# Kernel optimization log

Measured on AMD Instinct MI355X. Metric: run time of the kernel, lower is better.

Reference implementation:

```python
import jax, jax.numpy as jnp
import numpy as np

B, L, H, HKV, D, E = 2, 2048, 8, 1, 256, 2048
SCALING = D ** -0.5


def rotate_half(x):
    x1, x2 = jnp.split(x, 2, axis=-1)
    return jnp.concatenate([-x2, x1], axis=-1)


def setup_inputs() -> dict:
    key = jax.random.key(0)
    ks = jax.random.split(key, 5)
    hidden_states = jax.random.normal(ks[0], (B, L, E), jnp.float32)
    attention_mask = jnp.zeros((B, 1, 1, L, L), jnp.float32)  # additive mask (all visible)
    # standard RoPE tables, shape [L, D]
    inv_freq = 1.0 / (10000.0 ** (jnp.arange(0, D, 2, dtype=jnp.float32) / D))
    freqs = jnp.arange(L, dtype=jnp.float32)[:, None] * inv_freq[None, :]
    emb = jnp.concatenate([freqs, freqs], axis=-1)
    cos, sin = jnp.cos(emb), jnp.sin(emb)
    s = 0.02
    Wq = jax.random.normal(ks[1], (H * D, E), jnp.float32) * s
    Wk = jax.random.normal(ks[2], (HKV * D, E), jnp.float32) * s
    Wv = jax.random.normal(ks[3], (HKV * D, E), jnp.float32) * s
    Wo = jax.random.normal(ks[4], (E, H * D), jnp.float32) * s
    return {"hidden_states": hidden_states, "attention_mask": attention_mask,
            "cos": cos, "sin": sin, "Wq": Wq, "Wk": Wk, "Wv": Wv, "Wo": Wo}


def reference(hidden_states, attention_mask, cos, sin, Wq, Wk, Wv, Wo):
    b, l, _ = hidden_states.shape
    q = jnp.einsum('ble,de->bld', hidden_states, Wq)
    k = jnp.einsum('ble,de->bld', hidden_states, Wk)
    v = jnp.einsum('ble,de->bld', hidden_states, Wv)
    # q: [B, L, 1, H, D] -> transpose(1,3) -> [B, H, 1, L, D]
    q = jnp.transpose(q.reshape(b, l, 1, H, D), (0, 3, 2, 1, 4))
    # k, v: [B, 1, L, Hkv, D] -> transpose(2,3) -> [B, 1, Hkv, L, D]
    k = jnp.transpose(k.reshape(b, 1, l, HKV, D), (0, 1, 3, 2, 4))
    v = jnp.transpose(v.reshape(b, 1, l, HKV, D), (0, 1, 3, 2, 4))
    # RoPE (cos/sin broadcast over leading dims)
    q = q * cos + rotate_half(q) * sin
    k = k * cos + rotate_half(k) * sin
    # scores: [B, H, Hkv, L, L]
    attn = jnp.matmul(q, jnp.swapaxes(k, -1, -2)) * SCALING
    attn = attn + attention_mask
    attn = jax.nn.softmax(attn.astype(jnp.float32), axis=-1)
    out = jnp.matmul(attn, v)                         # [B, H, Hkv, L, D]
    out = jnp.transpose(out, (0, 1, 3, 2, 4))         # [B, H, L, Hkv, D]
    out = out.reshape(b, l, H * D)                    # row-major reshape, as torch .reshape
    return jnp.einsum('bld,ed->ble', out, Wo)
```

## Files before the change

### kernel.cpp

```cpp
#include <hip/hip_runtime.h>

typedef unsigned short u16;
typedef __attribute__((ext_vector_type(8))) short short8;
typedef __attribute__((ext_vector_type(4))) float f32x4;
typedef __attribute__((ext_vector_type(16))) float f32x16;

struct __align__(8) US4 { u16 x, y, z, w; };

__device__ __forceinline__ u16 f2bf(float x) {
  union { float f; unsigned u; } c; c.f = x;
  unsigned r = c.u + 0x7fffu + ((c.u >> 16) & 1u);
  return (u16)(r >> 16);
}
__device__ __forceinline__ float bf2f(u16 u) {
  union { unsigned u; float f; } c; c.u = ((unsigned)u) << 16;
  return c.f;
}
__device__ __forceinline__ void gload_lds16(const void* g, void* l) {
  __builtin_amdgcn_global_load_lds(
      (const __attribute__((address_space(1))) void*)g,
      (__attribute__((address_space(3))) void*)l, 16, 0, 0);
}
__device__ __forceinline__ f32x4 fzero4() {
  f32x4 z; z[0] = 0.f; z[1] = 0.f; z[2] = 0.f; z[3] = 0.f; return z;
}

__global__ __launch_bounds__(256) void cvt_all(
    const float* __restrict__ h, const float* __restrict__ wq,
    const float* __restrict__ wk, const float* __restrict__ wv,
    const float* __restrict__ wo, u16* __restrict__ Xbf,
    u16* __restrict__ Wqkv, u16* __restrict__ Wob) {
  int b = blockIdx.x;
  const float* s; u16* d; int off;
  if (b < 8192)       { s = h;  d = Xbf;            off = b; }
  else if (b < 12288) { s = wq; d = Wqkv;           off = b - 8192; }
  else if (b < 12800) { s = wk; d = Wqkv + 4194304; off = b - 12288; }
  else if (b < 13312) { s = wv; d = Wqkv + 4718592; off = b - 12800; }
  else                { s = wo; d = Wob;            off = b - 13312; }
  int i = (off * 256 + threadIdx.x) * 4;
  float4 v = *(const float4*)(s + i);
  US4 o = { f2bf(v.x), f2bf(v.y), f2bf(v.z), f2bf(v.w) };
  *(US4*)(d + i) = o;
}

template <int MODE>
__global__ __launch_bounds__(256) void gemm_nt(
    const u16* __restrict__ A, const u16* __restrict__ Bw,
    u16* __restrict__ q_out, u16* __restrict__ k_out, u16* __restrict__ v_out,
    float* __restrict__ c_out) {
  __shared__ u16 lA[128 * 32];
  __shared__ u16 lB[128 * 32];
  const int K = 2048;
  int t = threadIdx.x, w = t >> 6, lane = t & 63;
  int wm = w >> 1, wn = w & 1;
  int m0 = blockIdx.x * 128, n0 = blockIdx.y * 128;
  int g = lane >> 4, qi = lane & 15;

  f32x4 acc[4][4];
#pragma unroll
  for (int i = 0; i < 4; i++)
#pragma unroll
    for (int j = 0; j < 4; j++) acc[i][j] = fzero4();

  for (int k0 = 0; k0 < K; k0 += 32) {
#pragma unroll
    for (int i = 0; i < 2; i++) {
      int off = i * 4096 + w * 1024 + lane * 16;
      int row = off >> 6, cg = (off >> 4) & 3;
      gload_lds16(A + (size_t)(m0 + row) * K + k0 + cg * 8,
                  (char*)lA + i * 4096 + w * 1024);
      gload_lds16(Bw + (size_t)(n0 + row) * K + k0 + cg * 8,
                  (char*)lB + i * 4096 + w * 1024);
    }
    __syncthreads();
    short8 af[4], bfr[4];
#pragma unroll
    for (int f = 0; f < 4; f++) {
      int ra = wm * 64 + f * 16 + qi;
      int rb = wn * 64 + f * 16 + qi;
      int kb2 = g * 16;
      af[f] = *(const short8*)((const char*)lA + ra * 64 + kb2);
      bfr[f] = *(const short8*)((const char*)lB + rb * 64 + kb2);
    }
#pragma unroll
    for (int i = 0; i < 4; i++)
#pragma unroll
      for (int j = 0; j < 4; j++)
        acc[i][j] = __builtin_amdgcn_mfma_f32_16x16x32_bf16(af[i], bfr[j], acc[i][j], 0, 0, 0);
    __syncthreads();
  }

#pragma unroll
  for (int i = 0; i < 4; i++) {
#pragma unroll
    for (int j = 0; j < 4; j++) {
#pragma unroll
      for (int r = 0; r < 4; r++) {
        int m = m0 + wm * 64 + i * 16 + g * 4 + r;
        int n = n0 + wn * 64 + j * 16 + qi;
        float v = acc[i][j][r];
        if (MODE == 0) {
          int b = m >> 11, l = m & 2047;
          if (n < 2048) {
            int hh = n >> 8, dd = n & 255;
            q_out[(((size_t)(b * 8 + hh) * 2048) + l) * 256 + dd] = f2bf(v);
          } else if (n < 2304) {
            int dd = n - 2048;
            k_out[((size_t)b * 2048 + l) * 256 + dd] = f2bf(v);
          } else {
            int dd = n - 2304;
            v_out[((size_t)b * 256 + dd) * 2048 + l] = f2bf(v);
          }
        } else {
          c_out[(size_t)m * 2048 + n] = v;
        }
      }
    }
  }
}

__global__ __launch_bounds__(256) void rope_kernel(u16* __restrict__ q, u16* __restrict__ k,
                                                   const float* __restrict__ cosT,
                                                   const float* __restrict__ sinT) {
  int idx = blockIdx.x * 2 + (threadIdx.x >> 7);
  int d = threadIdx.x & 127;
  u16* ptr;
  int l;
  float sc;
  if (idx < 32768) { ptr = q + (size_t)idx * 256; l = idx & 2047; sc = 0.0625f; }
  else             { ptr = k + (size_t)(idx - 32768) * 256; l = (idx - 32768) & 2047; sc = 1.0f; }
  float x1 = bf2f(ptr[d]), x2 = bf2f(ptr[d + 128]);
  float c1 = cosT[l * 256 + d], s1 = sinT[l * 256 + d];
  float c2 = cosT[l * 256 + d + 128], s2 = sinT[l * 256 + d + 128];
  float o1 = (x1 * c1 - x2 * s1) * sc;
  float o2 = (x2 * c2 + x1 * s2) * sc;
  ptr[d] = f2bf(o1);
  ptr[d + 128] = f2bf(o2);
}

__global__ __launch_bounds__(512, 2) void flash_kernel(
    const u16* __restrict__ qr, const u16* __restrict__ kr,
    const u16* __restrict__ vt_g, u16* __restrict__ attnout) {
  __shared__ __align__(16) char lds[147456];

  int t = threadIdx.x, w = t >> 6, lane = t & 63;
  int lo5 = lane & 31, hi = lane >> 5;
  int half = w >> 2, wl = w & 3;
  int b = blockIdx.z, h = blockIdx.y;
  int bh = b * 8 + h;
  int l0 = blockIdx.x * 128;
  int qrow = l0 + wl * 32 + lo5;

  const u16* kb = kr + (size_t)b * (2048 * 256);
  const u16* vb = vt_g + (size_t)b * (256 * 2048);
  char* unitbase = lds + half * 65536;
  char* plw = lds + 131072 + w * 2048;
  int kvbase = half * 1024;

  short8 qf[16];
  {
    const u16* qb = qr + ((size_t)bh * 2048 + qrow) * 256 + hi * 8;
#pragma unroll
    for (int ks = 0; ks < 16; ks++) qf[ks] = *(const short8*)(qb + ks * 16);
  }

  f32x16 ot[8];
#pragma unroll
  for (int dv = 0; dv < 8; dv++)
#pragma unroll
    for (int r = 0; r < 16; r++) ot[dv][r] = 0.f;
  float mrow = -1e30f, lrow = 0.f;

  auto stage = [&](int buf, int it) {
    char* unit = unitbase + buf * 32768;
    int kvg = kvbase + it * 32;
#pragma unroll
    for (int i = 0; i < 4; i++) {
      int dbase = i * 4096 + wl * 1024;
      int off = dbase + lane * 16;
      {
        int row = off >> 9, slot = (off >> 4) & 31;
        int ss = slot ^ (row & 7);
        gload_lds16(kb + (size_t)(kvg + row) * 256 + ss * 8, unit + dbase);
      }
      {
        int dd = off >> 6, slot = (off >> 4) & 3;
        int ss = slot ^ ((dd >> 1) & 3);
        gload_lds16(vb + (size_t)dd * 2048 + kvg + ss * 8, unit + 16384 + dbase);
      }
    }
  };

  stage(0, 0);
  __syncthreads();

  for (int it = 0; it < 32; ++it) {
    int buf = it & 1;
    if (it < 31) stage(buf ^ 1, it + 1);
    char* unit = unitbase + buf * 32768;

    f32x16 st;
#pragma unroll
    for (int r = 0; r < 16; r++) st[r] = 0.f;
#pragma unroll
    for (int ks = 0; ks < 16; ks++) {
      int ss = (2 * ks + hi) ^ (lo5 & 7);
      short8 kf = *(const short8*)(unit + lo5 * 512 + ss * 16);
      st = __builtin_amdgcn_mfma_f32_32x32x16_bf16(kf, qf[ks], st, 0, 0, 0);
    }

    float tmax = st[0];
#pragma unroll
    for (int r = 1; r < 16; r++) tmax = fmaxf(tmax, st[r]);
    tmax = fmaxf(tmax, __shfl_xor(tmax, 32));
    if (__any(tmax > mrow)) {
      float mnew = fmaxf(mrow, tmax);
      float scale = __expf(mrow - mnew);
#pragma unroll
      for (int dv = 0; dv < 8; dv++)
#pragma unroll
        for (int r = 0; r < 16; r++) ot[dv][r] *= scale;
      lrow *= scale;
      mrow = mnew;
    }
    float tsum = 0.f;
#pragma unroll
    for (int r = 0; r < 16; r++) {
      float p = __expf(st[r] - mrow);
      st[r] = p;
      tsum += p;
    }
    tsum += __shfl_xor(tsum, 32);
    lrow += tsum;

#pragma unroll
    for (int r4 = 0; r4 < 4; r4++) {
      US4 pw = { f2bf(st[4 * r4 + 0]), f2bf(st[4 * r4 + 1]),
                 f2bf(st[4 * r4 + 2]), f2bf(st[4 * r4 + 3]) };
      int byte_ = lo5 * 64 + ((r4 ^ ((lo5 >> 1) & 3)) << 4) + hi * 8;
      *(US4*)(plw + byte_) = pw;
    }

#pragma unroll
    for (int jks = 0; jks < 2; jks++) {
      int ps = ((2 * jks + hi) ^ ((lo5 >> 1) & 3)) << 4;
      short8 pf = *(const short8*)(plw + lo5 * 64 + ps);
#pragma unroll
      for (int dv = 0; dv < 8; dv++) {
        int dd = dv * 32 + lo5;
        int ss = (2 * jks + hi) ^ ((dd >> 1) & 3);
        short8 vf = *(const short8*)(unit + 16384 + dd * 64 + ss * 16);
        ot[dv] = __builtin_amdgcn_mfma_f32_32x32x16_bf16(vf, pf, ot[dv], 0, 0, 0);
      }
    }
    __syncthreads();
  }

  char* chunk = lds + wl * 32768;
  float* mlx = (float*)(lds + 131072 + wl * 4096);
  if (half == 0) {
#pragma unroll
    for (int dv = 0; dv < 8; dv++)
#pragma unroll
      for (int r4 = 0; r4 < 4; r4++) {
        f32x4 v;
        v[0] = ot[dv][4 * r4 + 0]; v[1] = ot[dv][4 * r4 + 1];
        v[2] = ot[dv][4 * r4 + 2]; v[3] = ot[dv][4 * r4 + 3];
        *(f32x4*)(chunk + ((dv * 4 + r4) * 64 + lane) * 16) = v;
      }
    mlx[lane * 2 + 0] = mrow;
    mlx[lane * 2 + 1] = lrow;
  }
  __syncthreads();
  if (half == 1) {
    float mA = mlx[lane * 2 + 0], lA = mlx[lane * 2 + 1];
    float m = fmaxf(mA, mrow);
    float cA = __expf(mA - m), cB = __expf(mrow - m);
    float linv = 1.f / (lA * cA + lrow * cB);
    u16* ob = attnout + ((size_t)bh * 2048 + qrow) * 256;
#pragma unroll
    for (int dv = 0; dv < 8; dv++)
#pragma unroll
      for (int r4 = 0; r4 < 4; r4++) {
        f32x4 oA = *(const f32x4*)(chunk + ((dv * 4 + r4) * 64 + lane) * 16);
        US4 o;
        o.x = f2bf((oA[0] * cA + ot[dv][4 * r4 + 0] * cB) * linv);
        o.y = f2bf((oA[1] * cA + ot[dv][4 * r4 + 1] * cB) * linv);
        o.z = f2bf((oA[2] * cA + ot[dv][4 * r4 + 2] * cB) * linv);
        o.w = f2bf((oA[3] * cA + ot[dv][4 * r4 + 3] * cB) * linv);
        *(US4*)(ob + dv * 32 + 8 * r4 + 4 * hi) = o;
      }
  }
}

extern "C" void kernel_launch(void* const* d_in, const int* in_sizes, int n_in,
                              void* d_out, int out_size, void* d_ws, size_t ws_size,
                              hipStream_t stream) {
  const float* hidden = (const float*)d_in[0];
  const float* cosT = (const float*)d_in[2];
  const float* sinT = (const float*)d_in[3];
  const float* Wq = (const float*)d_in[4];
  const float* Wk = (const float*)d_in[5];
  const float* Wv = (const float*)d_in[6];
  const float* Wo = (const float*)d_in[7];

  char* ws = (char*)d_ws;
  u16* Xbf  = (u16*)(ws + 0);
  u16* Wqkv = (u16*)(ws + 16777216);
  u16* Wob  = (u16*)(ws + 27262976);
  u16* qbuf = (u16*)(ws + 35651584);
  u16* kbuf = (u16*)(ws + 52428800);
  u16* vT   = (u16*)(ws + 54525952);
  u16* attn = (u16*)(ws + 56623104);
  float* out = (float*)d_out;

  cvt_all<<<17408, 256, 0, stream>>>(hidden, Wq, Wk, Wv, Wo, Xbf, Wqkv, Wob);
  gemm_nt<0><<<dim3(32, 20), 256, 0, stream>>>(Xbf, Wqkv, qbuf, kbuf, vT, nullptr);
  rope_kernel<<<18432, 256, 0, stream>>>(qbuf, kbuf, cosT, sinT);
  flash_kernel<<<dim3(16, 8, 2), 512, 0, stream>>>(qbuf, kbuf, vT, attn);
  gemm_nt<1><<<dim3(32, 16), 256, 0, stream>>>(attn, Wob, nullptr, nullptr, nullptr, out);
}
```

Baseline: 281.0 us.

## Give each flash wave two query tiles and keep P in registers

The flash kernel now runs 4 waves per block instead of 8, and each wave handles two 32-row query tiles. Every K and V fragment read from LDS therefore feeds two MFMAs. The probability tile is converted to bf16 with packed converts and rearranged across lanes using permlane32 swaps, replacing the LDS write/read round trip. It also raises wave priority around the MFMA loops. In exchange, each wave holds twice as many accumulators and Q fragments, which raises register pressure. There are also fewer waves available to hide latency, and occupancy is set to 1 block per CU.

```diff
diff --git a/kernel.cpp b/kernel.cpp
--- a/kernel.cpp
+++ b/kernel.cpp
@@ -23,6 +23,11 @@
 }
 __device__ __forceinline__ f32x4 fzero4() {
   f32x4 z; z[0] = 0.f; z[1] = 0.f; z[2] = 0.f; z[3] = 0.f; return z;
+}
+__device__ __forceinline__ unsigned cvtpk(float lo, float hi) {
+  unsigned r;
+  asm("v_cvt_pk_bf16_f32 %0, %1, %2" : "=v"(r) : "v"(lo), "v"(hi));
+  return r;
 }
 
 __global__ __launch_bounds__(256) void cvt_all(
@@ -138,55 +143,55 @@
   ptr[d + 128] = f2bf(o2);
 }
 
-__global__ __launch_bounds__(512, 2) void flash_kernel(
+__global__ __launch_bounds__(256, 1) void flash_kernel(
     const u16* __restrict__ qr, const u16* __restrict__ kr,
     const u16* __restrict__ vt_g, u16* __restrict__ attnout) {
-  __shared__ __align__(16) char lds[147456];
+  __shared__ __align__(16) char lds[132096];
 
   int t = threadIdx.x, w = t >> 6, lane = t & 63;
   int lo5 = lane & 31, hi = lane >> 5;
-  int half = w >> 2, wl = w & 3;
+  int half = w >> 1, ws = w & 1;
   int b = blockIdx.z, h = blockIdx.y;
   int bh = b * 8 + h;
   int l0 = blockIdx.x * 128;
-  int qrow = l0 + wl * 32 + lo5;
 
   const u16* kb = kr + (size_t)b * (2048 * 256);
   const u16* vb = vt_g + (size_t)b * (256 * 2048);
   char* unitbase = lds + half * 65536;
-  char* plw = lds + 131072 + w * 2048;
   int kvbase = half * 1024;
 
-  short8 qf[16];
+  short8 qf0[16], qf1[16];
   {
-    const u16* qb = qr + ((size_t)bh * 2048 + qrow) * 256 + hi * 8;
-#pragma unroll
-    for (int ks = 0; ks < 16; ks++) qf[ks] = *(const short8*)(qb + ks * 16);
-  }
-
-  f32x16 ot[8];
-#pragma unroll
-  for (int dv = 0; dv < 8; dv++)
-#pragma unroll
-    for (int r = 0; r < 16; r++) ot[dv][r] = 0.f;
-  float mrow = -1e30f, lrow = 0.f;
+    const u16* qb0 = qr + ((size_t)bh * 2048 + l0 + ws * 64 + lo5) * 256 + hi * 8;
+    const u16* qb1 = qb0 + 32 * 256;
+#pragma unroll
+    for (int ks = 0; ks < 16; ks++) {
+      qf0[ks] = *(const short8*)(qb0 + ks * 16);
+      qf1[ks] = *(const short8*)(qb1 + ks * 16);
+    }
+  }
+
+  f32x16 ot[16];
+#pragma unroll
+  for (int i = 0; i < 16; i++)
+#pragma unroll
+    for (int r = 0; r < 16; r++) ot[i][r] = 0.f;
+  float m0r = -1e30f, l0r = 0.f, m1r = -1e30f, l1r = 0.f;
 
   auto stage = [&](int buf, int it) {
     char* unit = unitbase + buf * 32768;
     int kvg = kvbase + it * 32;
 #pragma unroll
-    for (int i = 0; i < 4; i++) {
-      int dbase = i * 4096 + wl * 1024;
+    for (int i = 0; i < 8; i++) {
+      int dbase = (i * 2 + ws) * 1024;
       int off = dbase + lane * 16;
       {
-        int row = off >> 9, slot = (off >> 4) & 31;
-        int ss = slot ^ (row & 7);
-        gload_lds16(kb + (size_t)(kvg + row) * 256 + ss * 8, unit + dbase);
+        int row = off >> 9, slot = (off >> 4) & 31, ss2 = slot ^ (row & 7);
+        gload_lds16(kb + (size_t)(kvg + row) * 256 + ss2 * 8, unit + dbase);
       }
       {
-        int dd = off >> 6, slot = (off >> 4) & 3;
-        int ss = slot ^ ((dd >> 1) & 3);
-        gload_lds16(vb + (size_t)dd * 2048 + kvg + ss * 8, unit + 16384 + dbase);
+        int dd = off >> 6, slot = (off >> 4) & 3, ss2 = slot ^ ((dd >> 1) & 3);
+        gload_lds16(vb + (size_t)dd * 2048 + kvg + ss2 * 8, unit + 16384 + dbase);
       }
     }
   };
@@ -199,97 +204,148 @@
     if (it < 31) stage(buf ^ 1, it + 1);
     char* unit = unitbase + buf * 32768;
 
-    f32x16 st;
-#pragma unroll
-    for (int r = 0; r < 16; r++) st[r] = 0.f;
+    f32x16 st0, st1;
+#pragma unroll
+    for (int r = 0; r < 16; r++) { st0[r] = 0.f; st1[r] = 0.f; }
+    __builtin_amdgcn_s_setprio(1);
 #pragma unroll
     for (int ks = 0; ks < 16; ks++) {
       int ss = (2 * ks + hi) ^ (lo5 & 7);
       short8 kf = *(const short8*)(unit + lo5 * 512 + ss * 16);
-      st = __builtin_amdgcn_mfma_f32_32x32x16_bf16(kf, qf[ks], st, 0, 0, 0);
-    }
-
-    float tmax = st[0];
-#pragma unroll
-    for (int r = 1; r < 16; r++) tmax = fmaxf(tmax, st[r]);
-    tmax = fmaxf(tmax, __shfl_xor(tmax, 32));
-    if (__any(tmax > mrow)) {
-      float mnew = fmaxf(mrow, tmax);
-      float scale = __expf(mrow - mnew);
-#pragma unroll
-      for (int dv = 0; dv < 8; dv++)
-#pragma unroll
-        for (int r = 0; r < 16; r++) ot[dv][r] *= scale;
-      lrow *= scale;
-      mrow = mnew;
-    }
-    float tsum = 0.f;
-#pragma unroll
-    for (int r = 0; r < 16; r++) {
-      float p = __expf(st[r] - mrow);
-      st[r] = p;
-      tsum += p;
-    }
-    tsum += __shfl_xor(tsum, 32);
-    lrow += tsum;
-
-#pragma unroll
-    for (int r4 = 0; r4 < 4; r4++) {
-      US4 pw = { f2bf(st[4 * r4 + 0]), f2bf(st[4 * r4 + 1]),
-                 f2bf(st[4 * r4 + 2]), f2bf(st[4 * r4 + 3]) };
-      int byte_ = lo5 * 64 + ((r4 ^ ((lo5 >> 1) & 3)) << 4) + hi * 8;
-      *(US4*)(plw + byte_) = pw;
+      st0 = __builtin_amdgcn_mfma_f32_32x32x16_bf16(kf, qf0[ks], st0, 0, 0, 0);
+      st1 = __builtin_amdgcn_mfma_f32_32x32x16_bf16(kf, qf1[ks], st1, 0, 0, 0);
+    }
+    __builtin_amdgcn_s_setprio(0);
+
+    {
+      float tmax = st0[0];
+#pragma unroll
+      for (int r = 1; r < 16; r++) tmax = fmaxf(tmax, st0[r]);
+      tmax = fmaxf(tmax, __shfl_xor(tmax, 32));
+      if (__any(tmax > m0r)) {
+        float mnew = fmaxf(m0r, tmax);
+        float sc = __expf(m0r - mnew);
+#pragma unroll
+        for (int dv = 0; dv < 8; dv++)
+#pragma unroll
+          for (int r = 0; r < 16; r++) ot[dv][r] *= sc;
+        l0r *= sc; m0r = mnew;
+      }
+      float ts = 0.f;
+#pragma unroll
+      for (int r = 0; r < 16; r++) {
+        float p = __expf(st0[r] - m0r);
+        st0[r] = p; ts += p;
+      }
+      ts += __shfl_xor(ts, 32);
+      l0r += ts;
+    }
+    {
+      float tmax = st1[0];
+#pragma unroll
+      for (int r = 1; r < 16; r++) tmax = fmaxf(tmax, st1[r]);
+      tmax = fmaxf(tmax, __shfl_xor(tmax, 32));
+      if (__any(tmax > m1r)) {
+        float mnew = fmaxf(m1r, tmax);
+        float sc = __expf(m1r - mnew);
+#pragma unroll
+        for (int dv = 0; dv < 8; dv++)
+#pragma unroll
+          for (int r = 0; r < 16; r++) ot[8 + dv][r] *= sc;
+        l1r *= sc; m1r = mnew;
+      }
+      float ts = 0.f;
+#pragma unroll
+      for (int r = 0; r < 16; r++) {
+        float p = __expf(st1[r] - m1r);
+        st1[r] = p; ts += p;
+      }
+      ts += __shfl_xor(ts, 32);
+      l1r += ts;
     }
 
 #pragma unroll
     for (int jks = 0; jks < 2; jks++) {
-      int ps = ((2 * jks + hi) ^ ((lo5 >> 1) & 3)) << 4;
-      short8 pf = *(const short8*)(plw + lo5 * 64 + ps);
+      union { unsigned u[4]; short8 s; } pf0u, pf1u;
+      {
+        unsigned a0 = cvtpk(st0[8 * jks + 0], st0[8 * jks + 1]);
+        unsigned a1 = cvtpk(st0[8 * jks + 2], st0[8 * jks + 3]);
+        unsigned b0 = cvtpk(st0[8 * jks + 4], st0[8 * jks + 5]);
+        unsigned b1 = cvtpk(st0[8 * jks + 6], st0[8 * jks + 7]);
+        asm("v_permlane32_swap_b32 %0, %1" : "+v"(a0), "+v"(b0));
+        asm("v_permlane32_swap_b32 %0, %1" : "+v"(a1), "+v"(b1));
+        pf0u.u[0] = a0; pf0u.u[1] = a1; pf0u.u[2] = b0; pf0u.u[3] = b1;
+      }
+      {
+        unsigned a0 = cvtpk(st1[8 * jks + 0], st1[8 * jks + 1]);
+        unsigned a1 = cvtpk(st1[8 * jks + 2], st1[8 * jks + 3]);
+        unsigned b0 = cvtpk(st1[8 * jks + 4], st1[8 * jks + 5]);
+        unsigned b1 = cvtpk(st1[8 * jks + 6], st1[8 * jks + 7]);
+        asm("v_permlane32_swap_b32 %0, %1" : "+v"(a0), "+v"(b0));
+        asm("v_permlane32_swap_b32 %0, %1" : "+v"(a1), "+v"(b1));
+        pf1u.u[0] = a0; pf1u.u[1] = a1; pf1u.u[2] = b0; pf1u.u[3] = b1;
+      }
+      short8 pf0 = pf0u.s, pf1 = pf1u.s;
+      __builtin_amdgcn_s_setprio(1);
 #pragma unroll
       for (int dv = 0; dv < 8; dv++) {
         int dd = dv * 32 + lo5;
         int ss = (2 * jks + hi) ^ ((dd >> 1) & 3);
         short8 vf = *(const short8*)(unit + 16384 + dd * 64 + ss * 16);
-        ot[dv] = __builtin_amdgcn_mfma_f32_32x32x16_bf16(vf, pf, ot[dv], 0, 0, 0);
-      }
+        ot[dv]     = __builtin_amdgcn_mfma_f32_32x32x16_bf16(vf, pf0, ot[dv], 0, 0, 0);
+        ot[8 + dv] = __builtin_amdgcn_mfma_f32_32x32x16_bf16(vf, pf1, ot[8 + dv], 0, 0, 0);
+      }
+      __builtin_amdgcn_s_setprio(0);
     }
     __syncthreads();
   }
 
-  char* chunk = lds + wl * 32768;
-  float* mlx = (float*)(lds + 131072 + wl * 4096);
+  char* chunk = lds + ws * 65536;
+  float* mlx = (float*)(lds + 131072);
   if (half == 0) {
 #pragma unroll
-    for (int dv = 0; dv < 8; dv++)
-#pragma unroll
-      for (int r4 = 0; r4 < 4; r4++) {
-        f32x4 v;
-        v[0] = ot[dv][4 * r4 + 0]; v[1] = ot[dv][4 * r4 + 1];
-        v[2] = ot[dv][4 * r4 + 2]; v[3] = ot[dv][4 * r4 + 3];
-        *(f32x4*)(chunk + ((dv * 4 + r4) * 64 + lane) * 16) = v;
-      }
-    mlx[lane * 2 + 0] = mrow;
-    mlx[lane * 2 + 1] = lrow;
+    for (int qg = 0; qg < 2; qg++)
+#pragma unroll
+      for (int dv = 0; dv < 8; dv++)
+#pragma unroll
+        for (int r4 = 0; r4 < 4; r4++) {
+          f32x4 v;
+          v[0] = ot[qg * 8 + dv][4 * r4 + 0]; v[1] = ot[qg * 8 + dv][4 * r4 + 1];
+          v[2] = ot[qg * 8 + dv][4 * r4 + 2]; v[3] = ot[qg * 8 + dv][4 * r4 + 3];
+          *(f32x4*)(chunk + (((qg * 8 + dv) * 4 + r4) * 64 + lane) * 16) = v;
+        }
+    if (hi == 0) {
+      mlx[((ws * 2 + 0) * 32 + lo5) * 2 + 0] = m0r;
+      mlx[((ws * 2 + 0) * 32 + lo5) * 2 + 1] = l0r;
+      mlx[((ws * 2 + 1) * 32 + lo5) * 2 + 0] = m1r;
+      mlx[((ws * 2 + 1) * 32 + lo5) * 2 + 1] = l1r;
+    }
   }
   __syncthreads();
   if (half == 1) {
-    float mA = mlx[lane * 2 + 0], lA = mlx[lane * 2 + 1];
-    float m = fmaxf(mA, mrow);
-    float cA = __expf(mA - m), cB = __expf(mrow - m);
-    float linv = 1.f / (lA * cA + lrow * cB);
-    u16* ob = attnout + ((size_t)bh * 2048 + qrow) * 256;
-#pragma unroll
-    for (int dv = 0; dv < 8; dv++)
-#pragma unroll
-      for (int r4 = 0; r4 < 4; r4++) {
-        f32x4 oA = *(const f32x4*)(chunk + ((dv * 4 + r4) * 64 + lane) * 16);
-        US4 o;
-        o.x = f2bf((oA[0] * cA + ot[dv][4 * r4 + 0] * cB) * linv);
-        o.y = f2bf((oA[1] * cA + ot[dv][4 * r4 + 1] * cB) * linv);
-        o.z = f2bf((oA[2] * cA + ot[dv][4 * r4 + 2] * cB) * linv);
-        o.w = f2bf((oA[3] * cA + ot[dv][4 * r4 + 3] * cB) * linv);
-        *(US4*)(ob + dv * 32 + 8 * r4 + 4 * hi) = o;
-      }
+#pragma unroll
+    for (int qg = 0; qg < 2; qg++) {
+      float mA = mlx[((ws * 2 + qg) * 32 + lo5) * 2 + 0];
+      float lA = mlx[((ws * 2 + qg) * 32 + lo5) * 2 + 1];
+      float mB = qg ? m1r : m0r;
+      float lB = qg ? l1r : l0r;
+      float m = fmaxf(mA, mB);
+      float cA = __expf(mA - m), cB = __expf(mB - m);
+      float linv = 1.f / (lA * cA + lB * cB);
+      u16* ob = attnout + ((size_t)bh * 2048 + l0 + ws * 64 + qg * 32 + lo5) * 256;
+#pragma unroll
+      for (int dv = 0; dv < 8; dv++)
+#pragma unroll
+        for (int r4 = 0; r4 < 4; r4++) {
+          f32x4 oA = *(const f32x4*)(chunk + (((qg * 8 + dv) * 4 + r4) * 64 + lane) * 16);
+          US4 o;
+          o.x = f2bf((oA[0] * cA + ot[qg * 8 + dv][4 * r4 + 0] * cB) * linv);
+          o.y = f2bf((oA[1] * cA + ot[qg * 8 + dv][4 * r4 + 1] * cB) * linv);
+          o.z = f2bf((oA[2] * cA + ot[qg * 8 + dv][4 * r4 + 2] * cB) * linv);
+          o.w = f2bf((oA[3] * cA + ot[qg * 8 + dv][4 * r4 + 3] * cB) * linv);
+          *(US4*)(ob + dv * 32 + 8 * r4 + 4 * hi) = o;
+        }
+    }
   }
 }
 
@@ -317,6 +373,6 @@
   cvt_all<<<17408, 256, 0, stream>>>(hidden, Wq, Wk, Wv, Wo, Xbf, Wqkv, Wob);
   gemm_nt<0><<<dim3(32, 20), 256, 0, stream>>>(Xbf, Wqkv, qbuf, kbuf, vT, nullptr);
   rope_kernel<<<18432, 256, 0, stream>>>(qbuf, kbuf, cosT, sinT);
-  flash_kernel<<<dim3(16, 8, 2), 512, 0, stream>>>(qbuf, kbuf, vT, attn);
+  flash_kernel<<<dim3(16, 8, 2), 256, 0, stream>>>(qbuf, kbuf, vT, attn);
   gemm_nt<1><<<dim3(32, 16), 256, 0, stream>>>(attn, Wob, nullptr, nullptr, nullptr, out);
 }
```

After: 815.7 us. 2.9x slower.
